# Performance work log

Measured on AMD Instinct MI355X. Metric: run time of the kernel, lower is better.

The kernel has to match this reference:

```python
import jax, jax.numpy as jnp
import numpy as np

N, B, D, A, E, H = 8, 32768, 128, 64, 32, 128


def setup_inputs() -> dict:
    key = jax.random.key(0)
    ks = jax.random.split(key, 22)
    g = lambda k, shape: (jax.random.normal(k, shape, dtype=jnp.float32) * 0.1)
    return {
        "states": jax.random.normal(ks[0], (N, B, D), dtype=jnp.float32),
        # per-agent DQN (2-hidden-layer MLP), stacked over agents
        "W1": g(ks[1], (N, D, H)), "b1": g(ks[2], (N, H)),
        "W2": g(ks[3], (N, H, H)), "b2": g(ks[4], (N, H)),
        "W3": g(ks[5], (N, H, A)), "b3": g(ks[6], (N, A)),
        # per-agent query MLP
        "Wq1": g(ks[7], (N, D, E)), "bq1": g(ks[8], (N, E)),
        "Wq2": g(ks[9], (N, E, E)), "bq2": g(ks[10], (N, E)),
        # per-agent key Linear
        "Wk": g(ks[11], (N, D, E)), "bk": g(ks[12], (N, E)),
        # shared scaling MLP (D->1->1)
        "Ws1": g(ks[13], (D, 1)), "bs1": g(ks[14], (1,)),
        "Ws2": g(ks[15], (1, 1)), "bs2": g(ks[16], (1,)),
        # shared constraint MLP (D->E->1)
        "Wc1": g(ks[17], (D, E)), "bc1": g(ks[18], (E,)),
        "Wc2": g(ks[19], (E, 1)), "bc2": g(ks[20], (1,)),
    }


def reference(states, W1, b1, W2, b2, W3, b3, Wq1, bq1, Wq2, bq2, Wk, bk,
              Ws1, bs1, Ws2, bs2, Wc1, bc1, Wc2, bc2):
    relu = jax.nn.relu
    # per-agent DQN -> q_values [B, N, A]
    h = relu(jnp.einsum('nbd,ndh->nbh', states, W1) + b1[:, None, :])
    h = relu(jnp.einsum('nbh,nhk->nbk', h, W2) + b2[:, None, :])
    q_values = (jnp.einsum('nbh,nha->nba', h, W3) + b3[:, None, :]).transpose(1, 0, 2)
    # per-agent keys [B, N, E]
    keys = (jnp.einsum('nbd,nde->nbe', states, Wk) + bk[:, None, :]).transpose(1, 0, 2)
    # per-agent queries [B, N, E]
    qh = relu(jnp.einsum('nbd,nde->nbe', states, Wq1) + bq1[:, None, :])
    queries = (jnp.einsum('nbe,nef->nbf', qh, Wq2) + bq2[:, None, :]).transpose(1, 0, 2)
    # attention [B, N, N]
    scores = jnp.einsum('bnd,bmd->bnm', queries, keys) / jnp.sqrt(jnp.float32(E))
    attn = jax.nn.softmax(scores, axis=-1)
    # faithful to original einsum 'bnm,bna->bna' (sums attn over m)
    weighted_qs = jnp.einsum('bnm,bna->bna', attn, q_values)
    # shared scaling MLP, sigmoid gate [B, N, 1]
    s = relu(jnp.einsum('nbd,do->nbo', states, Ws1) + bs1)
    s = jnp.einsum('nbo,op->nbp', s, Ws2) + bs2
    scaling = jax.nn.sigmoid(s.transpose(1, 0, 2))
    summed_q = jnp.mean(scaling * weighted_qs, axis=1)  # [B, A]
    # shared constraint MLP [B, N, 1] -> mean over agents [B, 1]
    c = relu(jnp.einsum('nbd,de->nbe', states, Wc1) + bc1)
    c = (jnp.einsum('nbe,eo->nbo', c, Wc2) + bc2).transpose(1, 0, 2)
    c = jnp.mean(c, axis=1)
    return summed_q + c  # [B, A]
```

## Files before the change

### kernel.cpp

```cpp
#include <hip/hip_runtime.h>
#include <hip/hip_bf16.h>

#define NAG 8
#define BATCH 32768
#define DDIM 128
#define ADIM 64
#define HDIM 128

#define NJ1 11
#define NJ2 8
#define NJ3 4
#define FB_L1 (NJ1*4)
#define FB_L2 (NJ2*4)
#define FB_L3 (NJ3*4)
#define FB_TOT (FB_L1+FB_L2+FB_L3)
#define WAGENT (FB_TOT*512)
#define NV_L1 (FB_L1*64)
#define NV_L23 ((FB_L2+FB_L3)*64)

typedef __attribute__((ext_vector_type(8))) short bf16x8;
typedef __attribute__((ext_vector_type(4))) float f32x4;
typedef __attribute__((ext_vector_type(4))) unsigned int u32x4;

static __device__ __forceinline__ unsigned short f2bf(float f) {
  unsigned int u = __builtin_bit_cast(unsigned int, f);
  u += 0x7fffu + ((u >> 16) & 1u);
  return (unsigned short)(u >> 16);
}

static __device__ __forceinline__ unsigned int cvt_pk_bf16(float a, float b) {
  unsigned int r;
  asm("v_cvt_pk_bf16_f32 %0, %1, %2" : "=v"(r) : "v"(a), "v"(b));
  return r;
}

__global__ void __launch_bounds__(256)
prep_weights(const float* __restrict__ W1, const float* __restrict__ W2,
             const float* __restrict__ W3, const float* __restrict__ Wc1,
             const float* __restrict__ Ws1, const float* __restrict__ b1,
             const float* __restrict__ bc1, const float* __restrict__ bs1,
             unsigned short* __restrict__ wbuf, float* __restrict__ b1e)
{
  int tid = blockIdx.x * 256 + threadIdx.x;
  if (tid < NAG * WAGENT) {
    int agent = tid / WAGENT;
    int rem   = tid % WAGENT;
    int fb = rem >> 9;
    int li = rem & 511;
    int l = li >> 3, t = li & 7;
    int lr = l & 15, lg = l >> 4;
    float v = 0.0f;
    if (fb < FB_L1) {
      int j = fb >> 2, kk = fb & 3;
      int col = j*16 + lr, k = kk*32 + lg*8 + t;
      if (col < 128)       v = W1[((size_t)agent*128 + k)*128 + col];
      else if (col < 160)  v = Wc1[k*32 + (col-128)];
      else if (col == 160) v = Ws1[k];
    } else if (fb < FB_L1 + FB_L2) {
      int f = fb - FB_L1;
      int j = f >> 2, kk = f & 3;
      int col = j*16 + lr, k = kk*32 + lg*8 + t;
      v = W2[((size_t)agent*128 + k)*128 + col];
    } else {
      int f = fb - FB_L1 - FB_L2;
      int j = f >> 2, kk = f & 3;
      int col = j*16 + lr, k = kk*32 + lg*8 + t;
      v = W3[((size_t)agent*128 + k)*64 + col];
    }
    wbuf[tid] = f2bf(v);
  }
  if (tid < NAG * 176) {
    int agent = tid / 176, col = tid % 176;
    float v = 0.0f;
    if (col < 128)       v = b1[agent*128 + col];
    else if (col < 160)  v = bc1[col - 128];
    else if (col == 160) v = bs1[0];
    b1e[tid] = v;
  }
}

__global__ void __launch_bounds__(512, 1)
qatten_main(const float* __restrict__ states,
            const float* __restrict__ b2g, const float* __restrict__ b3g,
            const float* __restrict__ ws2p, const float* __restrict__ bs2p,
            const float* __restrict__ wc2g, const float* __restrict__ bc2p,
            const unsigned short* __restrict__ wbuf,
            const float* __restrict__ b1e,
            float* __restrict__ out)
{
  __shared__ __align__(16) unsigned short bufA[FB_L1*512];
  __shared__ __align__(16) unsigned short bufB[(FB_L2+FB_L3)*512];
  __shared__ __align__(16) unsigned short hlds[8 * 2048];

  const int tid  = threadIdx.x;
  const int wave = tid >> 6;
  const int lane = tid & 63;
  const int lr   = lane & 15;
  const int lg   = lane >> 4;
  const int row0 = blockIdx.x * 128 + wave * 16;

  unsigned short* hp = hlds + wave * 2048;

  const float ws2  = ws2p[0];
  const float bs2v = bs2p[0];
  const float bc2v = bc2p[0];
  const float wc2a = wc2g[lr];
  const float wc2b = wc2g[16 + lr];

  const f32x4 zero4 = {0.f, 0.f, 0.f, 0.f};

  f32x4 out_acc[NJ3];
#pragma unroll
  for (int j = 0; j < NJ3; ++j) out_acc[j] = zero4;

  {
    const u32x4* gA = (const u32x4*)wbuf;
    u32x4* lA = (u32x4*)bufA;
#pragma unroll
    for (int i = 0; i < 6; ++i) {
      int idx = tid + i*512;
      if (idx < NV_L1) lA[idx] = gA[idx];
    }
    const u32x4* gB = (const u32x4*)(wbuf + FB_L1*512);
    u32x4* lB = (u32x4*)bufB;
#pragma unroll
    for (int i = 0; i < 6; ++i)
      lB[tid + i*512] = gB[tid + i*512];
  }
  __syncthreads();

  u32x4 stg[6];

  for (int a = 0; a < NAG; ++a) {
    float b1v[NJ1], b2v[NJ2], b3v[NJ3];
#pragma unroll
    for (int j = 0; j < NJ1; ++j) b1v[j] = b1e[a*176 + j*16 + lr];
#pragma unroll
    for (int j = 0; j < NJ2; ++j) b2v[j] = b2g[a*HDIM + j*16 + lr];
#pragma unroll
    for (int j = 0; j < NJ3; ++j) b3v[j] = b3g[a*ADIM + j*16 + lr];

    bf16x8 afr[4];
    {
      const float* sb = states + ((size_t)a * BATCH + row0) * DDIM;
#pragma unroll
      for (int kk = 0; kk < 4; ++kk) {
        const float* p = sb + lr*DDIM + kk*32 + lg*8;
        f32x4 v0 = *(const f32x4*)p;
        f32x4 v1 = *(const f32x4*)(p + 4);
        u32x4 w;
        w[0] = cvt_pk_bf16(v0[0], v0[1]);
        w[1] = cvt_pk_bf16(v0[2], v0[3]);
        w[2] = cvt_pk_bf16(v1[0], v1[1]);
        w[3] = cvt_pk_bf16(v1[2], v1[3]);
        afr[kk] = __builtin_bit_cast(bf16x8, w);
      }
    }

    float scl[4], crow[4];
    {
      f32x4 eacc[3];
#pragma unroll
      for (int jx = 0; jx < 3; ++jx) {
        bf16x8 bfr[4];
#pragma unroll
        for (int kk = 0; kk < 4; ++kk)
          bfr[kk] = *(const bf16x8*)&bufA[((8+jx)*4 + kk)*512 + lane*8];
        f32x4 acc = zero4;
#pragma unroll
        for (int kk = 0; kk < 4; ++kk)
          acc = __builtin_amdgcn_mfma_f32_16x16x32_bf16(afr[kk], bfr[kk], acc, 0, 0, 0);
        eacc[jx] = acc;
      }
#pragma unroll
      for (int r = 0; r < 4; ++r) {
        float c0 = eacc[0][r] + b1v[8];  c0 = c0 > 0.f ? c0 : 0.f;
        float c1 = eacc[1][r] + b1v[9];  c1 = c1 > 0.f ? c1 : 0.f;
        float cd = c0*wc2a + c1*wc2b;
        cd += __shfl_xor(cd, 1);
        cd += __shfl_xor(cd, 2);
        cd += __shfl_xor(cd, 4);
        cd += __shfl_xor(cd, 8);
        crow[r] = cd + bc2v;
        float sp = eacc[2][r] + b1v[10];
        sp = __shfl(sp, lane & 48);
        sp = sp > 0.f ? sp : 0.f;
        float s = ws2 * sp + bs2v;
        scl[r] = 1.f / (1.f + __expf(-s));
      }
    }

#pragma unroll
    for (int j = 0; j < 8; ++j) {
      bf16x8 bfr[4];
#pragma unroll
      for (int kk = 0; kk < 4; ++kk)
        bfr[kk] = *(const bf16x8*)&bufA[(j*4 + kk)*512 + lane*8];
      f32x4 acc = zero4;
#pragma unroll
      for (int kk = 0; kk < 4; ++kk)
        acc = __builtin_amdgcn_mfma_f32_16x16x32_bf16(afr[kk], bfr[kk], acc, 0, 0, 0);
#pragma unroll
      for (int r = 0; r < 4; ++r) {
        float hv = acc[r] + b1v[j];
        hv = hv > 0.f ? hv : 0.f;
        int row = lg*4 + r;
        int bo = row*256 + (((j*16 + lr)*2) ^ ((row & 7) << 4));
        *(unsigned short*)((char*)hp + bo) = f2bf(hv);
      }
    }

    asm volatile("s_waitcnt lgkmcnt(0)" ::: "memory");
#pragma unroll
    for (int kk = 0; kk < 4; ++kk) {
      int row = lr;
      int bo = row*256 + ((kk*64 + lg*16) ^ ((row & 7) << 4));
      afr[kk] = *(const bf16x8*)((char*)hp + bo);
    }

    if (a > 0) {
      u32x4* lB = (u32x4*)bufB;
#pragma unroll
      for (int i = 0; i < 6; ++i)
        lB[tid + i*512] = stg[i];
    }
    __syncthreads();

    if (a < NAG-1) {
      const u32x4* g = (const u32x4*)(wbuf + (size_t)(a+1)*WAGENT);
#pragma unroll
      for (int i = 0; i < 6; ++i) {
        int idx = tid + i*512;
        if (idx < NV_L1) stg[i] = g[idx];
      }
    }

#pragma unroll
    for (int j = 0; j < 8; ++j) {
      bf16x8 bfr[4];
#pragma unroll
      for (int kk = 0; kk < 4; ++kk)
        bfr[kk] = *(const bf16x8*)&bufB[(j*4 + kk)*512 + lane*8];
      f32x4 acc = zero4;
#pragma unroll
      for (int kk = 0; kk < 4; ++kk)
        acc = __builtin_amdgcn_mfma_f32_16x16x32_bf16(afr[kk], bfr[kk], acc, 0, 0, 0);
#pragma unroll
      for (int r = 0; r < 4; ++r) {
        float hv = acc[r] + b2v[j];
        hv = hv > 0.f ? hv : 0.f;
        int row = lg*4 + r;
        int bo = row*256 + (((j*16 + lr)*2) ^ ((row & 7) << 4));
        *(unsigned short*)((char*)hp + bo) = f2bf(hv);
      }
    }

    asm volatile("s_waitcnt lgkmcnt(0)" ::: "memory");
#pragma unroll
    for (int kk = 0; kk < 4; ++kk) {
      int row = lr;
      int bo = row*256 + ((kk*64 + lg*16) ^ ((row & 7) << 4));
      afr[kk] = *(const bf16x8*)((char*)hp + bo);
    }

#pragma unroll
    for (int j = 0; j < NJ3; ++j) {
      bf16x8 bfr[4];
#pragma unroll
      for (int kk = 0; kk < 4; ++kk)
        bfr[kk] = *(const bf16x8*)&bufB[(FB_L2 + j*4 + kk)*512 + lane*8];
      f32x4 acc = zero4;
#pragma unroll
      for (int kk = 0; kk < 4; ++kk)
        acc = __builtin_amdgcn_mfma_f32_16x16x32_bf16(afr[kk], bfr[kk], acc, 0, 0, 0);
#pragma unroll
      for (int r = 0; r < 4; ++r)
        out_acc[j][r] += scl[r] * (acc[r] + b3v[j]) + crow[r];
    }

    if (a < NAG-1) {
      u32x4* lA = (u32x4*)bufA;
#pragma unroll
      for (int i = 0; i < 6; ++i) {
        int idx = tid + i*512;
        if (idx < NV_L1) lA[idx] = stg[i];
      }
    }
    __syncthreads();

    if (a < NAG-1) {
      const u32x4* g = (const u32x4*)(wbuf + (size_t)(a+1)*WAGENT + FB_L1*512);
#pragma unroll
      for (int i = 0; i < 6; ++i)
        stg[i] = g[tid + i*512];
    }
  }

#pragma unroll
  for (int j = 0; j < NJ3; ++j)
#pragma unroll
    for (int r = 0; r < 4; ++r) {
      size_t row = (size_t)row0 + lg*4 + r;
      out[row*ADIM + j*16 + lr] = out_acc[j][r] * 0.125f;
    }
}

extern "C" void kernel_launch(void* const* d_in, const int* in_sizes, int n_in,
                              void* d_out, int out_size, void* d_ws, size_t ws_size,
                              hipStream_t stream)
{
  const float* states = (const float*)d_in[0];
  const float* W1  = (const float*)d_in[1];
  const float* b1  = (const float*)d_in[2];
  const float* W2  = (const float*)d_in[3];
  const float* b2  = (const float*)d_in[4];
  const float* W3  = (const float*)d_in[5];
  const float* b3  = (const float*)d_in[6];
  const float* Ws1 = (const float*)d_in[13];
  const float* bs1 = (const float*)d_in[14];
  const float* Ws2 = (const float*)d_in[15];
  const float* bs2 = (const float*)d_in[16];
  const float* Wc1 = (const float*)d_in[17];
  const float* bc1 = (const float*)d_in[18];
  const float* Wc2 = (const float*)d_in[19];
  const float* bc2 = (const float*)d_in[20];

  unsigned short* wbuf = (unsigned short*)d_ws;
  float* b1e = (float*)((char*)d_ws + (size_t)NAG * WAGENT * 2);

  dim3 pb(256), pg((NAG * WAGENT + 255) / 256);
  prep_weights<<<pg, pb, 0, stream>>>(W1, W2, W3, Wc1, Ws1, b1, bc1, bs1, wbuf, b1e);

  dim3 mb(512), mg(BATCH / 128);
  qatten_main<<<mg, mb, 0, stream>>>(states, b2, b3, Ws2, bs2, Wc2, bc2,
                                     wbuf, b1e, (float*)d_out);
}
```

Baseline: 67.23 us.

## Stream weights directly into LDS via async loads and double-buffer B-fragment reads

```diff
diff --git a/kernel.cpp b/kernel.cpp
--- a/kernel.cpp
+++ b/kernel.cpp
@@ -13,10 +13,9 @@
 #define FB_L1 (NJ1*4)
 #define FB_L2 (NJ2*4)
 #define FB_L3 (NJ3*4)
+#define FB_B  (FB_L2+FB_L3)
 #define FB_TOT (FB_L1+FB_L2+FB_L3)
 #define WAGENT (FB_TOT*512)
-#define NV_L1 (FB_L1*64)
-#define NV_L23 ((FB_L2+FB_L3)*64)
 
 typedef __attribute__((ext_vector_type(8))) short bf16x8;
 typedef __attribute__((ext_vector_type(4))) float f32x4;
@@ -32,6 +31,12 @@
   unsigned int r;
   asm("v_cvt_pk_bf16_f32 %0, %1, %2" : "=v"(r) : "v"(a), "v"(b));
   return r;
+}
+
+static __device__ __forceinline__ void gload_lds16(const void* g, void* l) {
+  __builtin_amdgcn_global_load_lds(
+      (const __attribute__((address_space(1))) unsigned int*)g,
+      (__attribute__((address_space(3))) unsigned int*)l, 16, 0, 0);
 }
 
 __global__ void __launch_bounds__(256)
@@ -89,7 +94,7 @@
             float* __restrict__ out)
 {
   __shared__ __align__(16) unsigned short bufA[FB_L1*512];
-  __shared__ __align__(16) unsigned short bufB[(FB_L2+FB_L3)*512];
+  __shared__ __align__(16) unsigned short bufB[FB_B*512];
   __shared__ __align__(16) unsigned short hlds[8 * 2048];
 
   const int tid  = threadIdx.x;
@@ -114,22 +119,14 @@
   for (int j = 0; j < NJ3; ++j) out_acc[j] = zero4;
 
   {
-    const u32x4* gA = (const u32x4*)wbuf;
-    u32x4* lA = (u32x4*)bufA;
-#pragma unroll
-    for (int i = 0; i < 6; ++i) {
-      int idx = tid + i*512;
-      if (idx < NV_L1) lA[idx] = gA[idx];
-    }
-    const u32x4* gB = (const u32x4*)(wbuf + FB_L1*512);
-    u32x4* lB = (u32x4*)bufB;
-#pragma unroll
-    for (int i = 0; i < 6; ++i)
-      lB[tid + i*512] = gB[tid + i*512];
+    const char* sA = (const char*)wbuf;
+    for (int c = wave; c < FB_L1; c += 8)
+      gload_lds16(sA + c*1024 + lane*16, (char*)bufA + c*1024);
+    const char* sB = (const char*)(wbuf + FB_L1*512);
+    for (int c = wave; c < FB_B; c += 8)
+      gload_lds16(sB + c*1024 + lane*16, (char*)bufB + c*1024);
   }
   __syncthreads();
-
-  u32x4 stg[6];
 
   for (int a = 0; a < NAG; ++a) {
     float b1v[NJ1], b2v[NJ2], b3v[NJ3];
@@ -157,60 +154,64 @@
       }
     }
 
+    f32x4 eacc[3];
+    {
+      bf16x8 pf[2][4];
+#pragma unroll
+      for (int kk = 0; kk < 4; ++kk)
+        pf[0][kk] = *(const bf16x8*)&bufA[kk*512 + lane*8];
+#pragma unroll
+      for (int j = 0; j < 11; ++j) {
+        if (j < 10) {
+#pragma unroll
+          for (int kk = 0; kk < 4; ++kk)
+            pf[(j+1)&1][kk] = *(const bf16x8*)&bufA[((j+1)*4 + kk)*512 + lane*8];
+        }
+        f32x4 acc = zero4;
+#pragma unroll
+        for (int kk = 0; kk < 4; ++kk)
+          acc = __builtin_amdgcn_mfma_f32_16x16x32_bf16(afr[kk], pf[j&1][kk], acc, 0, 0, 0);
+        if (j < 8) {
+#pragma unroll
+          for (int r = 0; r < 4; ++r) {
+            float hv = acc[r] + b1v[j];
+            hv = hv > 0.f ? hv : 0.f;
+            int row = lg*4 + r;
+            int bo = row*256 + (((j*16 + lr)*2) ^ ((row & 7) << 4));
+            *(unsigned short*)((char*)hp + bo) = f2bf(hv);
+          }
+        } else {
+          eacc[j-8] = acc;
+        }
+      }
+    }
+
     float scl[4], crow[4];
-    {
-      f32x4 eacc[3];
-#pragma unroll
-      for (int jx = 0; jx < 3; ++jx) {
-        bf16x8 bfr[4];
-#pragma unroll
-        for (int kk = 0; kk < 4; ++kk)
-          bfr[kk] = *(const bf16x8*)&bufA[((8+jx)*4 + kk)*512 + lane*8];
-        f32x4 acc = zero4;
-#pragma unroll
-        for (int kk = 0; kk < 4; ++kk)
-          acc = __builtin_amdgcn_mfma_f32_16x16x32_bf16(afr[kk], bfr[kk], acc, 0, 0, 0);
-        eacc[jx] = acc;
-      }
-#pragma unroll
-      for (int r = 0; r < 4; ++r) {
-        float c0 = eacc[0][r] + b1v[8];  c0 = c0 > 0.f ? c0 : 0.f;
-        float c1 = eacc[1][r] + b1v[9];  c1 = c1 > 0.f ? c1 : 0.f;
-        float cd = c0*wc2a + c1*wc2b;
-        cd += __shfl_xor(cd, 1);
-        cd += __shfl_xor(cd, 2);
-        cd += __shfl_xor(cd, 4);
-        cd += __shfl_xor(cd, 8);
-        crow[r] = cd + bc2v;
-        float sp = eacc[2][r] + b1v[10];
-        sp = __shfl(sp, lane & 48);
-        sp = sp > 0.f ? sp : 0.f;
-        float s = ws2 * sp + bs2v;
-        scl[r] = 1.f / (1.f + __expf(-s));
-      }
-    }
-
-#pragma unroll
-    for (int j = 0; j < 8; ++j) {
-      bf16x8 bfr[4];
-#pragma unroll
-      for (int kk = 0; kk < 4; ++kk)
-        bfr[kk] = *(const bf16x8*)&bufA[(j*4 + kk)*512 + lane*8];
-      f32x4 acc = zero4;
-#pragma unroll
-      for (int kk = 0; kk < 4; ++kk)
-        acc = __builtin_amdgcn_mfma_f32_16x16x32_bf16(afr[kk], bfr[kk], acc, 0, 0, 0);
-#pragma unroll
-      for (int r = 0; r < 4; ++r) {
-        float hv = acc[r] + b1v[j];
-        hv = hv > 0.f ? hv : 0.f;
-        int row = lg*4 + r;
-        int bo = row*256 + (((j*16 + lr)*2) ^ ((row & 7) << 4));
-        *(unsigned short*)((char*)hp + bo) = f2bf(hv);
-      }
-    }
-
-    asm volatile("s_waitcnt lgkmcnt(0)" ::: "memory");
+#pragma unroll
+    for (int r = 0; r < 4; ++r) {
+      float c0 = eacc[0][r] + b1v[8];  c0 = c0 > 0.f ? c0 : 0.f;
+      float c1 = eacc[1][r] + b1v[9];  c1 = c1 > 0.f ? c1 : 0.f;
+      float cd = c0*wc2a + c1*wc2b;
+      cd += __shfl_xor(cd, 1);
+      cd += __shfl_xor(cd, 2);
+      cd += __shfl_xor(cd, 4);
+      cd += __shfl_xor(cd, 8);
+      crow[r] = cd + bc2v;
+      float sp = eacc[2][r] + b1v[10];
+      sp = __shfl(sp, lane & 48);
+      sp = sp > 0.f ? sp : 0.f;
+      float s = ws2 * sp + bs2v;
+      scl[r] = 1.f / (1.f + __expf(-s));
+    }
+
+    __syncthreads();
+
+    if (a < NAG-1) {
+      const char* sA = (const char*)(wbuf + (size_t)(a+1)*WAGENT);
+      for (int c = wave; c < FB_L1; c += 8)
+        gload_lds16(sA + c*1024 + lane*16, (char*)bufA + c*1024);
+    }
+
 #pragma unroll
     for (int kk = 0; kk < 4; ++kk) {
       int row = lr;
@@ -218,44 +219,33 @@
       afr[kk] = *(const bf16x8*)((char*)hp + bo);
     }
 
-    if (a > 0) {
-      u32x4* lB = (u32x4*)bufB;
-#pragma unroll
-      for (int i = 0; i < 6; ++i)
-        lB[tid + i*512] = stg[i];
-    }
-    __syncthreads();
-
-    if (a < NAG-1) {
-      const u32x4* g = (const u32x4*)(wbuf + (size_t)(a+1)*WAGENT);
-#pragma unroll
-      for (int i = 0; i < 6; ++i) {
-        int idx = tid + i*512;
-        if (idx < NV_L1) stg[i] = g[idx];
+    {
+      bf16x8 pf[2][4];
+#pragma unroll
+      for (int kk = 0; kk < 4; ++kk)
+        pf[0][kk] = *(const bf16x8*)&bufB[kk*512 + lane*8];
+#pragma unroll
+      for (int j = 0; j < 8; ++j) {
+        if (j < 7) {
+#pragma unroll
+          for (int kk = 0; kk < 4; ++kk)
+            pf[(j+1)&1][kk] = *(const bf16x8*)&bufB[((j+1)*4 + kk)*512 + lane*8];
+        }
+        f32x4 acc = zero4;
+#pragma unroll
+        for (int kk = 0; kk < 4; ++kk)
+          acc = __builtin_amdgcn_mfma_f32_16x16x32_bf16(afr[kk], pf[j&1][kk], acc, 0, 0, 0);
+#pragma unroll
+        for (int r = 0; r < 4; ++r) {
+          float hv = acc[r] + b2v[j];
+          hv = hv > 0.f ? hv : 0.f;
+          int row = lg*4 + r;
+          int bo = row*256 + (((j*16 + lr)*2) ^ ((row & 7) << 4));
+          *(unsigned short*)((char*)hp + bo) = f2bf(hv);
+        }
       }
     }
 
-#pragma unroll
-    for (int j = 0; j < 8; ++j) {
-      bf16x8 bfr[4];
-#pragma unroll
-      for (int kk = 0; kk < 4; ++kk)
-        bfr[kk] = *(const bf16x8*)&bufB[(j*4 + kk)*512 + lane*8];
-      f32x4 acc = zero4;
-#pragma unroll
-      for (int kk = 0; kk < 4; ++kk)
-        acc = __builtin_amdgcn_mfma_f32_16x16x32_bf16(afr[kk], bfr[kk], acc, 0, 0, 0);
-#pragma unroll
-      for (int r = 0; r < 4; ++r) {
-        float hv = acc[r] + b2v[j];
-        hv = hv > 0.f ? hv : 0.f;
-        int row = lg*4 + r;
-        int bo = row*256 + (((j*16 + lr)*2) ^ ((row & 7) << 4));
-        *(unsigned short*)((char*)hp + bo) = f2bf(hv);
-      }
-    }
-
-    asm volatile("s_waitcnt lgkmcnt(0)" ::: "memory");
 #pragma unroll
     for (int kk = 0; kk < 4; ++kk) {
       int row = lr;
@@ -263,36 +253,34 @@
       afr[kk] = *(const bf16x8*)((char*)hp + bo);
     }
 
-#pragma unroll
-    for (int j = 0; j < NJ3; ++j) {
-      bf16x8 bfr[4];
+    {
+      bf16x8 pf[2][4];
 #pragma unroll
       for (int kk = 0; kk < 4; ++kk)
-        bfr[kk] = *(const bf16x8*)&bufB[(FB_L2 + j*4 + kk)*512 + lane*8];
-      f32x4 acc = zero4;
-#pragma unroll
-      for (int kk = 0; kk < 4; ++kk)
-        acc = __builtin_amdgcn_mfma_f32_16x16x32_bf16(afr[kk], bfr[kk], acc, 0, 0, 0);
-#pragma unroll
-      for (int r = 0; r < 4; ++r)
-        out_acc[j][r] += scl[r] * (acc[r] + b3v[j]) + crow[r];
-    }
+        pf[0][kk] = *(const bf16x8*)&bufB[(FB_L2 + kk)*512 + lane*8];
+#pragma unroll
+      for (int j = 0; j < NJ3; ++j) {
+        if (j < NJ3-1) {
+#pragma unroll
+          for (int kk = 0; kk < 4; ++kk)
+            pf[(j+1)&1][kk] = *(const bf16x8*)&bufB[(FB_L2 + (j+1)*4 + kk)*512 + lane*8];
+        }
+        f32x4 acc = zero4;
+#pragma unroll
+        for (int kk = 0; kk < 4; ++kk)
+          acc = __builtin_amdgcn_mfma_f32_16x16x32_bf16(afr[kk], pf[j&1][kk], acc, 0, 0, 0);
+#pragma unroll
+        for (int r = 0; r < 4; ++r)
+          out_acc[j][r] += scl[r] * (acc[r] + b3v[j]) + crow[r];
+      }
+    }
+
+    __syncthreads();
 
     if (a < NAG-1) {
-      u32x4* lA = (u32x4*)bufA;
-#pragma unroll
-      for (int i = 0; i < 6; ++i) {
-        int idx = tid + i*512;
-        if (idx < NV_L1) lA[idx] = stg[i];
-      }
-    }
-    __syncthreads();
-
-    if (a < NAG-1) {
-      const u32x4* g = (const u32x4*)(wbuf + (size_t)(a+1)*WAGENT + FB_L1*512);
-#pragma unroll
-      for (int i = 0; i < 6; ++i)
-        stg[i] = g[tid + i*512];
+      const char* sB = (const char*)(wbuf + (size_t)(a+1)*WAGENT + FB_L1*512);
+      for (int c = wave; c < FB_B; c += 8)
+        gload_lds16(sB + c*1024 + lane*16, (char*)bufB + c*1024);
     }
   }
 
```

Result: faster. 65.36 us (-2.8%).
